# Kernel tuning notes

Hardware: AMD Instinct MI355X
Metric: run time of the kernel (lower is better)

Reference implementation:

```python
import jax, jax.numpy as jnp
import numpy as np

EPS = 0.1        # SinkhornDistance eps (hard-coded in SGE.__init__)
MAX_ITER = 10    # SinkhornDistance max_iter
THRESH = 0.1     # early-exit threshold in SinkhornDistance.forward
N_POINTS = 32
SPACE_DIM = 16   # emb_dim // n_points = 512 // 32


def _sinkhorn_cost(x, y):
    """Regularized OT cost between point clouds x, y: [B, P, D] -> [B]."""
    # C[b,i,j] = sum_d |x[b,i,d] - y[b,j,d]|^2
    C = jnp.sum(jnp.square(jnp.abs(x[:, :, None, :] - y[:, None, :, :])), axis=-1)
    B, P1 = x.shape[0], x.shape[1]
    P2 = y.shape[1]
    mu = jnp.full((B, P1), 1.0 / P1, dtype=x.dtype)
    nu = jnp.full((B, P2), 1.0 / P2, dtype=x.dtype)

    def M(u, v):
        # (-C + u_i + v_j) / eps
        return (-C + u[:, :, None] + v[:, None, :]) / EPS

    def step(carry, _):
        u, v, done = carry
        u_new = EPS * (jnp.log(mu + 1e-8) - jax.nn.logsumexp(M(u, v), axis=-1)) + u
        v_new = EPS * (jnp.log(nu + 1e-8)
                       - jax.nn.logsumexp(M(u_new, v).swapaxes(-2, -1), axis=-1)) + v
        err = jnp.mean(jnp.sum(jnp.abs(u_new - u), axis=-1))
        u2 = jnp.where(done, u, u_new)
        v2 = jnp.where(done, v, v_new)
        done2 = done | (err < THRESH)  # torch breaks AFTER applying the update
        return (u2, v2, done2), None

    init = (jnp.zeros_like(mu), jnp.zeros_like(nu), jnp.array(False))
    (u, v, _), _ = jax.lax.scan(step, init, None, length=MAX_ITER)
    pi = jnp.exp(M(u, v))
    return jnp.sum(pi * C, axis=(-2, -1))  # [B]


def setup_inputs() -> dict:
    key = jax.random.key(0)
    k1, k2, k3, k4 = jax.random.split(key, 4)
    n_nodes, feat, emb, n_edges = 10000, 256, 512, 4096
    x = jax.random.normal(k1, (n_nodes, feat), dtype=jnp.float32)
    W = jax.random.normal(k2, (feat, emb), dtype=jnp.float32) / np.float32(np.sqrt(feat))
    edges_pos = jax.random.randint(k3, (2, n_edges), 0, n_nodes)
    edges_neg = jax.random.randint(k4, (2, n_edges), 0, n_nodes)
    return {"x": x, "W": W, "edges_pos": edges_pos, "edges_neg": edges_neg}


def reference(x, W, edges_pos, edges_neg):
    z = x @ W  # encoder: linear projection [n_nodes, emb_dim]

    def score_pairs(nx, ny):
        a = z[nx].reshape(-1, N_POINTS, SPACE_DIM)
        b = z[ny].reshape(-1, N_POINTS, SPACE_DIM)
        return -_sinkhorn_cost(a, b)

    pos_energy = score_pairs(edges_pos[0], edges_pos[1])
    neg_energy = score_pairs(edges_neg[0], edges_neg[1])
    loss = jnp.mean(pos_energy ** 2 + jnp.exp(neg_energy))
    return loss
```

## Files before the change

### kernel.cpp

```cpp
#include <hip/hip_runtime.h>
#include <hip/hip_bf16.h>
#include <math.h>

#define N_POINTS 32
#define SPACE_DIM 16
#define EMB 512
#define THRESH 0.1f
#define MAX_ITER 10
#define KDIM 256

#define NEG10LOG2E -14.42695040888963f
#define EPS_LN2     0.0693147180559945f
#define LOGMU2     -4.99999953834f

typedef _Float16 half8 __attribute__((ext_vector_type(8)));
typedef _Float16 half4 __attribute__((ext_vector_type(4)));
typedef float floatx4 __attribute__((ext_vector_type(4)));

#define BSTRIDE 264

__global__ __launch_bounds__(256) void gemm_fused(
    const float* __restrict__ X, const float* __restrict__ W,
    float* __restrict__ Z, int M, int K, int N, unsigned* __restrict__ counter)
{
    (void)K;
    if (blockIdx.x == 0 && blockIdx.y == 0 && threadIdx.x == 0) counter[0] = 0u;

    __shared__ _Float16 Bs[64][BSTRIDE];

    int t = threadIdx.x;
    int n0 = blockIdx.y * 64;

    int wave = t >> 6;
    int lane = t & 63;
    int quad = lane >> 4;
    int l16 = lane & 15;

    int mrow = blockIdx.x * 64 + wave * 16 + l16;
    int msafe = mrow < M ? mrow : M - 1;
    const float4* xp = (const float4*)(X + (size_t)msafe * KDIM);

    float4 xr[16];
    #pragma unroll
    for (int kk = 0; kk < 8; ++kk) {
        xr[2 * kk]     = xp[kk * 8 + quad * 2];
        xr[2 * kk + 1] = xp[kk * 8 + quad * 2 + 1];
    }

    #pragma unroll
    for (int s = 0; s < 4; ++s) {
        int u = s * 256 + t;
        int nb = u & 15;
        int kb = u >> 4;
        float4 r0v = *(const float4*)&W[(size_t)(kb * 4 + 0) * N + n0 + nb * 4];
        float4 r1v = *(const float4*)&W[(size_t)(kb * 4 + 1) * N + n0 + nb * 4];
        float4 r2v = *(const float4*)&W[(size_t)(kb * 4 + 2) * N + n0 + nb * 4];
        float4 r3v = *(const float4*)&W[(size_t)(kb * 4 + 3) * N + n0 + nb * 4];
        float c0[4] = {r0v.x, r0v.y, r0v.z, r0v.w};
        float c1[4] = {r1v.x, r1v.y, r1v.z, r1v.w};
        float c2[4] = {r2v.x, r2v.y, r2v.z, r2v.w};
        float c3[4] = {r3v.x, r3v.y, r3v.z, r3v.w};
        #pragma unroll
        for (int c = 0; c < 4; ++c) {
            half4 h = {(_Float16)c0[c], (_Float16)c1[c],
                       (_Float16)c2[c], (_Float16)c3[c]};
            *(half4*)&Bs[nb * 4 + c][kb * 4] = h;
        }
    }
    __syncthreads();

    floatx4 acc[4] = {{0.f,0.f,0.f,0.f},{0.f,0.f,0.f,0.f},
                      {0.f,0.f,0.f,0.f},{0.f,0.f,0.f,0.f}};

    #pragma unroll
    for (int kk = 0; kk < 8; ++kk) {
        float4 lo = xr[2 * kk];
        float4 hi = xr[2 * kk + 1];
        half8 a = {(_Float16)lo.x, (_Float16)lo.y, (_Float16)lo.z, (_Float16)lo.w,
                   (_Float16)hi.x, (_Float16)hi.y, (_Float16)hi.z, (_Float16)hi.w};
        #pragma unroll
        for (int ct = 0; ct < 4; ++ct) {
            half8 b = *(const half8*)&Bs[ct * 16 + l16][kk * 32 + quad * 8];
            acc[ct] = __builtin_amdgcn_mfma_f32_16x16x32_f16(a, b, acc[ct], 0, 0, 0);
        }
    }

    int rbase = blockIdx.x * 64 + wave * 16 + quad * 4;
    #pragma unroll
    for (int ct = 0; ct < 4; ++ct) {
        int col = n0 + ct * 16 + l16;
        #pragma unroll
        for (int r = 0; r < 4; ++r) {
            int row = rbase + r;
            if (row < M) Z[(size_t)row * N + col] = acc[ct][r];
        }
    }
}

#define WPB 4

__global__ __launch_bounds__(256, 4) void sinkhorn_fused(
    const float* __restrict__ Z,
    const int* __restrict__ ep, const int* __restrict__ en,
    int nE,
    float* __restrict__ err_part,
    float* __restrict__ cost_all)
{
    __shared__ float shm[WPB][32 * 36];
    __shared__ float uvs[WPB][64];

    int tid = threadIdx.x;
    int wv = tid >> 6;
    int t = tid & 63;
    int b = blockIdx.x * WPB + wv;

    int side = (b >= nE) ? 1 : 0;
    int e = b - side * nE;
    const int* edges = side ? en : ep;
    int nx = edges[e];
    int ny = edges[e + nE];

    int c = t & 31;
    int h = t >> 5;
    int r0 = h * 16;

    float* sb  = shm[wv];
    float* csh = shm[wv];
    float* Ul  = uvs[wv];
    float* Vl  = uvs[wv] + 32;

    {
        const float4* zb4 = (const float4*)(Z + (size_t)ny * EMB);
        float4 q0 = zb4[t * 2];
        float4 q1 = zb4[t * 2 + 1];
        float* dst = sb + (t >> 1) * 20 + (t & 1) * 8;
        ((float4*)dst)[0] = q0;
        ((float4*)dst)[1] = q1;
    }
    float areg[16];
    {
        const float4* za4 = (const float4*)(Z + (size_t)nx * EMB + c * SPACE_DIM);
        float4 a0 = za4[0], a1 = za4[1], a2 = za4[2], a3 = za4[3];
        areg[0]=a0.x; areg[1]=a0.y; areg[2]=a0.z; areg[3]=a0.w;
        areg[4]=a1.x; areg[5]=a1.y; areg[6]=a1.z; areg[7]=a1.w;
        areg[8]=a2.x; areg[9]=a2.y; areg[10]=a2.z; areg[11]=a2.w;
        areg[12]=a3.x; areg[13]=a3.y; areg[14]=a3.z; areg[15]=a3.w;
    }

    float Crow[16];
    #pragma unroll
    for (int jj = 0; jj < 16; ++jj) {
        const float* bp = sb + (r0 + jj) * 20;
        float s = 0.f;
        #pragma unroll
        for (int d = 0; d < SPACE_DIM; ++d) {
            float diff = areg[d] - bp[d];
            s = fmaf(diff, diff, s);
        }
        Crow[jj] = s * NEG10LOG2E;
    }
    #pragma unroll
    for (int g = 0; g < 4; ++g) {
        *(float4*)&csh[c * 36 + r0 + g * 4] =
            make_float4(Crow[g*4+0], Crow[g*4+1], Crow[g*4+2], Crow[g*4+3]);
    }
    float Ccol[16];
    #pragma unroll
    for (int ii = 0; ii < 16; ++ii)
        Ccol[ii] = csh[(r0 + ii) * 36 + c];

    Vl[c] = 0.f;
    float U = 0.f;
    float ccp[MAX_ITER];
    float dup[MAX_ITER];

    #pragma unroll
    for (int it = 0; it < MAX_ITER; ++it) {
        float w[16];
        {
            const float4* vp = (const float4*)(Vl + r0);
            float4 v0 = vp[0], v1 = vp[1], v2 = vp[2], v3 = vp[3];
            float vv[16] = {v0.x,v0.y,v0.z,v0.w, v1.x,v1.y,v1.z,v1.w,
                            v2.x,v2.y,v2.z,v2.w, v3.x,v3.y,v3.z,v3.w};
            #pragma unroll
            for (int jj = 0; jj < 16; ++jj) w[jj] = Crow[jj] + vv[jj];
        }
        float m8[8];
        #pragma unroll
        for (int k = 0; k < 8; ++k) m8[k] = fmaxf(w[k], w[k + 8]);
        float m4a = fmaxf(m8[0], m8[4]), m4b = fmaxf(m8[1], m8[5]);
        float m4c = fmaxf(m8[2], m8[6]), m4d = fmaxf(m8[3], m8[7]);
        float mx = fmaxf(fmaxf(m4a, m4b), fmaxf(m4c, m4d));
        mx = fmaxf(mx, __shfl_xor(mx, 32));

        float ex[16];
        #pragma unroll
        for (int jj = 0; jj < 16; ++jj) ex[jj] = __builtin_amdgcn_exp2f(w[jj] - mx);
        float s8[8], p8[8];
        #pragma unroll
        for (int k = 0; k < 8; ++k) {
            s8[k] = ex[k] + ex[k + 8];
            p8[k] = fmaf(ex[k], Crow[k], ex[k + 8] * Crow[k + 8]);
        }
        float sm = ((s8[0]+s8[4]) + (s8[1]+s8[5])) + ((s8[2]+s8[6]) + (s8[3]+s8[7]));
        float pc = ((p8[0]+p8[4]) + (p8[1]+p8[5])) + ((p8[2]+p8[6]) + (p8[3]+p8[7]));
        sm += __shfl_xor(sm, 32);

        if (it > 0) ccp[it - 1] = __builtin_amdgcn_exp2f(U + mx) * pc;

        float Un = LOGMU2 - (mx + __builtin_amdgcn_logf(sm));
        dup[it] = fabsf(Un - U);
        U = Un;
        Ul[c] = U;

        float wc[16];
        {
            const float4* up = (const float4*)(Ul + r0);
            float4 u0 = up[0], u1 = up[1], u2 = up[2], u3 = up[3];
            float uu[16] = {u0.x,u0.y,u0.z,u0.w, u1.x,u1.y,u1.z,u1.w,
                            u2.x,u2.y,u2.z,u2.w, u3.x,u3.y,u3.z,u3.w};
            #pragma unroll
            for (int ii = 0; ii < 16; ++ii) wc[ii] = Ccol[ii] + uu[ii];
        }
        float n8[8];
        #pragma unroll
        for (int k = 0; k < 8; ++k) n8[k] = fmaxf(wc[k], wc[k + 8]);
        float n4a = fmaxf(n8[0], n8[4]), n4b = fmaxf(n8[1], n8[5]);
        float n4c = fmaxf(n8[2], n8[6]), n4d = fmaxf(n8[3], n8[7]);
        float mx2 = fmaxf(fmaxf(n4a, n4b), fmaxf(n4c, n4d));
        mx2 = fmaxf(mx2, __shfl_xor(mx2, 32));

        float e2[16];
        #pragma unroll
        for (int ii = 0; ii < 16; ++ii) e2[ii] = __builtin_amdgcn_exp2f(wc[ii] - mx2);
        float t8[8];
        #pragma unroll
        for (int k = 0; k < 8; ++k) t8[k] = e2[k] + e2[k + 8];
        float sm2 = ((t8[0]+t8[4]) + (t8[1]+t8[5])) + ((t8[2]+t8[6]) + (t8[3]+t8[7]));
        sm2 += __shfl_xor(sm2, 32);
        float Vn = LOGMU2 - (mx2 + __builtin_amdgcn_logf(sm2));
        Vl[c] = Vn;
    }

    {
        const float4* vp = (const float4*)(Vl + r0);
        float4 v0 = vp[0], v1 = vp[1], v2 = vp[2], v3 = vp[3];
        float vv[16] = {v0.x,v0.y,v0.z,v0.w, v1.x,v1.y,v1.z,v1.w,
                        v2.x,v2.y,v2.z,v2.w, v3.x,v3.y,v3.z,v3.w};
        float cc = 0.f;
        #pragma unroll
        for (int jj = 0; jj < 16; ++jj)
            cc = fmaf(__builtin_amdgcn_exp2f(U + Crow[jj] + vv[jj]), Crow[jj], cc);
        ccp[MAX_ITER - 1] = cc;
    }

    #pragma unroll
    for (int m = 1; m < 32; m <<= 1) {
        #pragma unroll
        for (int k = 0; k < MAX_ITER; ++k) {
            dup[k] += __shfl_xor(dup[k], m);
            ccp[k] += __shfl_xor(ccp[k], m);
        }
    }
    #pragma unroll
    for (int k = 0; k < MAX_ITER; ++k) ccp[k] += __shfl_xor(ccp[k], 32);

    if (t == 0) {
        #pragma unroll
        for (int k = 0; k < MAX_ITER; ++k)
            err_part[(size_t)k * (2 * nE) + b] = EPS_LN2 * dup[k];
        #pragma unroll
        for (int k = 0; k < MAX_ITER; ++k)
            cost_all[(size_t)k * (2 * nE) + b] = -EPS_LN2 * ccp[k];
    }
}

__global__ __launch_bounds__(256) void err_final(
    const float* __restrict__ err_part, const float* __restrict__ cost_all,
    float* __restrict__ err_mean, unsigned* __restrict__ counter,
    float* __restrict__ out, int nE)
{
    __shared__ float red[256];
    __shared__ int is_last;

    int side = blockIdx.x / MAX_ITER;
    int it = blockIdx.x - side * MAX_ITER;
    const float* p = err_part + (size_t)it * (2 * nE) + side * nE;
    float s = 0.f;
    for (int idx = threadIdx.x; idx < nE; idx += 256) s += p[idx];
    red[threadIdx.x] = s;
    __syncthreads();
    for (int stride = 128; stride > 0; stride >>= 1) {
        if (threadIdx.x < stride) red[threadIdx.x] += red[threadIdx.x + stride];
        __syncthreads();
    }
    if (threadIdx.x == 0) {
        __hip_atomic_store(&err_mean[side * MAX_ITER + it], red[0] / (float)nE,
                           __ATOMIC_RELAXED, __HIP_MEMORY_SCOPE_AGENT);
        __threadfence();
        unsigned old = __hip_atomic_fetch_add(counter, 1u, __ATOMIC_ACQ_REL,
                                              __HIP_MEMORY_SCOPE_AGENT);
        is_last = (old == 2 * MAX_ITER - 1);
    }
    __syncthreads();
    if (!is_last) return;

    float em[2 * MAX_ITER];
    #pragma unroll
    for (int i = 0; i < 2 * MAX_ITER; ++i)
        em[i] = __hip_atomic_load(&err_mean[i], __ATOMIC_RELAXED,
                                  __HIP_MEMORY_SCOPE_AGENT);
    int Tp = MAX_ITER, Tn = MAX_ITER;
    for (int i = 0; i < MAX_ITER; ++i)
        if (em[i] < THRESH) { Tp = i + 1; break; }
    for (int i = 0; i < MAX_ITER; ++i)
        if (em[MAX_ITER + i] < THRESH) { Tn = i + 1; break; }

    float acc = 0.f;
    for (int b = threadIdx.x; b < 2 * nE; b += 256) {
        int sd = (b >= nE) ? 1 : 0;
        int T = sd ? Tn : Tp;
        float cost = cost_all[(size_t)(T - 1) * (2 * nE) + b];
        acc += sd ? expf(-cost) : cost * cost;
    }
    __syncthreads();
    red[threadIdx.x] = acc;
    __syncthreads();
    for (int stride = 128; stride > 0; stride >>= 1) {
        if (threadIdx.x < stride) red[threadIdx.x] += red[threadIdx.x + stride];
        __syncthreads();
    }
    if (threadIdx.x == 0) out[0] = red[0] / (float)nE;
}

extern "C" void kernel_launch(void* const* d_in, const int* in_sizes, int n_in,
                              void* d_out, int out_size, void* d_ws, size_t ws_size,
                              hipStream_t stream)
{
    const float* X = (const float*)d_in[0];
    const float* W = (const float*)d_in[1];
    const int* ep = (const int*)d_in[2];
    const int* en = (const int*)d_in[3];
    float* out = (float*)d_out;

    int K = in_sizes[1] / EMB;
    int M = in_sizes[0] / K;
    int nE = in_sizes[2] / 2;

    float* ws = (float*)d_ws;
    float* Z = ws;
    float* err_part = Z + (size_t)M * EMB;
    float* cost_all = err_part + (size_t)MAX_ITER * 2 * nE;
    float* err_mean = cost_all + (size_t)MAX_ITER * 2 * nE;
    unsigned* counter = (unsigned*)(err_mean + 32);

    dim3 gg((M + 63) / 64, EMB / 64);
    gemm_fused<<<gg, 256, 0, stream>>>(X, W, Z, M, K, EMB, counter);

    int nblk = (2 * nE) / WPB;
    sinkhorn_fused<<<nblk, 64 * WPB, 0, stream>>>(Z, ep, en, nE, err_part, cost_all);

    err_final<<<2 * MAX_ITER, 256, 0, stream>>>(err_part, cost_all, err_mean,
                                                counter, out, nE);
}
```

Baseline: 148.1 us.

## Fold final error reduction and loss into sinkhorn kernel via last-block counter

Removes the separate err_final launch. Each sinkhorn block increments a global counter after writing its outputs, and the last block to arrive performs the per-iteration error means, picks the early-exit iteration, and reduces the loss. This saves one kernel launch and its dependency gap, but serializes the final reduction onto a single block. It also raises the occupancy hint in launch_bounds from 4 to 8, which may force register pressure or spills. The code relies on gemm_fused resetting the counter, as the earlier design did.

Measured after the change: 375.9 us. 2.54x slower.

```diff
diff --git a/kernel.cpp b/kernel.cpp
--- a/kernel.cpp
+++ b/kernel.cpp
@@ -99,12 +99,14 @@
 
 #define WPB 4
 
-__global__ __launch_bounds__(256, 4) void sinkhorn_fused(
+__global__ __launch_bounds__(256, 8) void sinkhorn_fused(
     const float* __restrict__ Z,
     const int* __restrict__ ep, const int* __restrict__ en,
     int nE,
     float* __restrict__ err_part,
-    float* __restrict__ cost_all)
+    float* __restrict__ cost_all,
+    unsigned* __restrict__ counter,
+    float* __restrict__ out)
 {
     __shared__ float shm[WPB][32 * 36];
     __shared__ float uvs[WPB][64];
@@ -273,64 +275,56 @@
         for (int k = 0; k < MAX_ITER; ++k)
             cost_all[(size_t)k * (2 * nE) + b] = -EPS_LN2 * ccp[k];
     }
-}
-
-__global__ __launch_bounds__(256) void err_final(
-    const float* __restrict__ err_part, const float* __restrict__ cost_all,
-    float* __restrict__ err_mean, unsigned* __restrict__ counter,
-    float* __restrict__ out, int nE)
-{
-    __shared__ float red[256];
-    __shared__ int is_last;
-
-    int side = blockIdx.x / MAX_ITER;
-    int it = blockIdx.x - side * MAX_ITER;
-    const float* p = err_part + (size_t)it * (2 * nE) + side * nE;
-    float s = 0.f;
-    for (int idx = threadIdx.x; idx < nE; idx += 256) s += p[idx];
-    red[threadIdx.x] = s;
-    __syncthreads();
-    for (int stride = 128; stride > 0; stride >>= 1) {
-        if (threadIdx.x < stride) red[threadIdx.x] += red[threadIdx.x + stride];
-        __syncthreads();
-    }
-    if (threadIdx.x == 0) {
-        __hip_atomic_store(&err_mean[side * MAX_ITER + it], red[0] / (float)nE,
-                           __ATOMIC_RELAXED, __HIP_MEMORY_SCOPE_AGENT);
+
+    float* sred = &shm[0][0];
+    float* em_s = sred + 256;
+    int*   isl  = (int*)(sred + 280);
+
+    __syncthreads();
+    if (tid == 0) {
         __threadfence();
         unsigned old = __hip_atomic_fetch_add(counter, 1u, __ATOMIC_ACQ_REL,
                                               __HIP_MEMORY_SCOPE_AGENT);
-        is_last = (old == 2 * MAX_ITER - 1);
-    }
-    __syncthreads();
-    if (!is_last) return;
-
-    float em[2 * MAX_ITER];
-    #pragma unroll
-    for (int i = 0; i < 2 * MAX_ITER; ++i)
-        em[i] = __hip_atomic_load(&err_mean[i], __ATOMIC_RELAXED,
-                                  __HIP_MEMORY_SCOPE_AGENT);
+        *isl = (old == gridDim.x - 1) ? 1 : 0;
+    }
+    __syncthreads();
+    if (!*isl) return;
+
+    #pragma unroll
+    for (int i = 0; i < 5; ++i) {
+        int r = wv * 5 + i;
+        int sd_ = r >= 10 ? 1 : 0;
+        int it_ = r - sd_ * 10;
+        const float* p = err_part + (size_t)it_ * (2 * nE) + (size_t)sd_ * nE;
+        float s = 0.f;
+        for (int idx = t; idx < nE; idx += 64) s += p[idx];
+        #pragma unroll
+        for (int m = 1; m < 64; m <<= 1) s += __shfl_xor(s, m);
+        if (t == 0) em_s[r] = s / (float)nE;
+    }
+    __syncthreads();
+
     int Tp = MAX_ITER, Tn = MAX_ITER;
     for (int i = 0; i < MAX_ITER; ++i)
-        if (em[i] < THRESH) { Tp = i + 1; break; }
+        if (em_s[i] < THRESH) { Tp = i + 1; break; }
     for (int i = 0; i < MAX_ITER; ++i)
-        if (em[MAX_ITER + i] < THRESH) { Tn = i + 1; break; }
+        if (em_s[10 + i] < THRESH) { Tn = i + 1; break; }
 
     float acc = 0.f;
-    for (int b = threadIdx.x; b < 2 * nE; b += 256) {
-        int sd = (b >= nE) ? 1 : 0;
+    for (int b2 = tid; b2 < 2 * nE; b2 += 256) {
+        int sd = (b2 >= nE) ? 1 : 0;
         int T = sd ? Tn : Tp;
-        float cost = cost_all[(size_t)(T - 1) * (2 * nE) + b];
+        float cost = cost_all[(size_t)(T - 1) * (2 * nE) + b2];
         acc += sd ? expf(-cost) : cost * cost;
     }
     __syncthreads();
-    red[threadIdx.x] = acc;
+    sred[tid] = acc;
     __syncthreads();
     for (int stride = 128; stride > 0; stride >>= 1) {
-        if (threadIdx.x < stride) red[threadIdx.x] += red[threadIdx.x + stride];
+        if (tid < stride) sred[tid] += sred[tid + stride];
         __syncthreads();
     }
-    if (threadIdx.x == 0) out[0] = red[0] / (float)nE;
+    if (tid == 0) out[0] = sred[0] / (float)nE;
 }
 
 extern "C" void kernel_launch(void* const* d_in, const int* in_sizes, int n_in,
@@ -351,15 +345,12 @@
     float* Z = ws;
     float* err_part = Z + (size_t)M * EMB;
     float* cost_all = err_part + (size_t)MAX_ITER * 2 * nE;
-    float* err_mean = cost_all + (size_t)MAX_ITER * 2 * nE;
-    unsigned* counter = (unsigned*)(err_mean + 32);
+    unsigned* counter = (unsigned*)(cost_all + (size_t)MAX_ITER * 2 * nE);
 
     dim3 gg((M + 63) / 64, EMB / 64);
     gemm_fused<<<gg, 256, 0, stream>>>(X, W, Z, M, K, EMB, counter);
 
     int nblk = (2 * nE) / WPB;
-    sinkhorn_fused<<<nblk, 64 * WPB, 0, stream>>>(Z, ep, en, nE, err_part, cost_all);
-
-    err_final<<<2 * MAX_ITER, 256, 0, stream>>>(err_part, cost_all, err_mean,
-                                                counter, out, nE);
+    sinkhorn_fused<<<nblk, 64 * WPB, 0, stream>>>(Z, ep, en, nE, err_part,
+                                                  cost_all, counter, out);
 }
```
